# Kernel tuning notes

Hardware: AMD Instinct MI355X
Metric: run time of the kernel (lower is better)

## Reference

```python
import jax, jax.numpy as jnp
import numpy as np

N, E, D, H, C, ED, G = 50000, 1000000, 128, 8, 16, 16, 8
HC = H * C  # = output_dim = 128
EPS = 1e-5
NEG_SLOPE = 0.2


def setup_inputs() -> dict:
    key = jax.random.key(0)
    ks = jax.random.split(key, 12)
    s = 1.0 / np.sqrt(D)
    inp = {
        "x": jax.random.normal(ks[0], (N, D), jnp.float32),
        "edge_index": jax.random.randint(ks[1], (2, E), 0, N, jnp.int64),
        "edge_attr": jax.random.normal(ks[2], (E, ED), jnp.float32),
        "batch": jnp.sort(jax.random.randint(ks[3], (N,), 0, G, jnp.int64)),
        # GATv2Conv params
        "Wl": jax.random.normal(ks[4], (D, HC), jnp.float32) * s,
        "bl": jnp.zeros((HC,), jnp.float32),
        "Wr": jax.random.normal(ks[5], (D, HC), jnp.float32) * s,
        "br": jnp.zeros((HC,), jnp.float32),
        "We": jax.random.normal(ks[6], (ED, HC), jnp.float32) * (1.0 / np.sqrt(ED)),
        "att": jax.random.normal(ks[7], (H, C), jnp.float32) * (1.0 / np.sqrt(C)),
        "bias": jnp.zeros((HC,), jnp.float32),
        # GraphNorm params
        "gn_weight": jnp.ones((HC,), jnp.float32),
        "gn_bias": jnp.zeros((HC,), jnp.float32),
        "gn_mean_scale": jnp.ones((HC,), jnp.float32),
    }
    return inp


def reference(x, edge_index, edge_attr, batch, Wl, bl, Wr, br, We, att, bias,
              gn_weight, gn_bias, gn_mean_scale):
    src, dst = edge_index[0], edge_index[1]

    # --- add self-loops with edge_attr fill_value='mean' (PyG default) ---
    deg = jax.ops.segment_sum(jnp.ones((E,), jnp.float32), dst, num_segments=N)
    ea_mean = jax.ops.segment_sum(edge_attr, dst, num_segments=N) / jnp.maximum(deg, 1.0)[:, None]
    loop = jnp.arange(N, dtype=src.dtype)
    src2 = jnp.concatenate([src, loop])          # [E+N]
    dst2 = jnp.concatenate([dst, loop])          # [E+N]
    ea2 = jnp.concatenate([edge_attr, ea_mean])  # [E+N, ED]

    # --- GATv2 attention ---
    xl = (x @ Wl + bl).reshape(N, H, C)  # source transform
    xr = (x @ Wr + br).reshape(N, H, C)  # target transform
    ee = (ea2 @ We).reshape(-1, H, C)
    m = xl[src2] + xr[dst2] + ee                              # [E+N, H, C]
    e = jnp.einsum('ehc,hc->eh', jax.nn.leaky_relu(m, NEG_SLOPE), att)  # [E+N, H]

    # segment softmax over destination nodes (every node has a self-loop)
    emax = jax.ops.segment_max(e, dst2, num_segments=N)       # [N, H]
    ex = jnp.exp(e - emax[dst2])
    denom = jax.ops.segment_sum(ex, dst2, num_segments=N)     # [N, H]
    alpha = ex / denom[dst2]                                  # [E+N, H]

    agg = jax.ops.segment_sum(alpha[:, :, None] * xl[src2], dst2, num_segments=N)
    out = agg.reshape(N, HC) + bias

    # residual (res_connection is Identity since input_dim == output_dim)
    out = out + x

    # --- GraphNorm over batch segments ---
    cnt = jax.ops.segment_sum(jnp.ones((N,), jnp.float32), batch, num_segments=G)
    cnt = jnp.maximum(cnt, 1.0)[:, None]
    mean = jax.ops.segment_sum(out, batch, num_segments=G) / cnt   # [G, HC]
    sub = out - gn_mean_scale * mean[batch]
    var = jax.ops.segment_sum(sub * sub, batch, num_segments=G) / cnt
    out = gn_weight * sub / jnp.sqrt(var[batch] + EPS) + gn_bias

    # ELU activation (dropout is identity in eval)
    return jax.nn.elu(out)
```

## Files before the change

### kernel.cpp

```cpp
#include <hip/hip_runtime.h>

#define HC 128
#define HEADS 8
#define EDIM 16
#define NG 8
#define GEPS 1e-5f
#define LOG2E 1.44269504f

typedef float f32x2 __attribute__((ext_vector_type(2)));

__device__ __forceinline__ unsigned pack_bf16x2(float a, float b) {
  unsigned ua = __float_as_uint(a), ub = __float_as_uint(b);
  ua = (ua + 0x7fffu + ((ua >> 16) & 1u)) >> 16;
  ub = (ub + 0x7fffu + ((ub >> 16) & 1u)) >> 16;
  return ua | (ub << 16);
}
__device__ __forceinline__ f32x2 unpack_bf16x2(unsigned u) {
  return (f32x2){__uint_as_float(u << 16), __uint_as_float(u & 0xffff0000u)};
}

__device__ __forceinline__ float head8_sum(float p) {
  int t;
  t = __builtin_amdgcn_update_dpp(0, __float_as_int(p), 0x141, 0xF, 0xF, true);
  p += __int_as_float(t);
  t = __builtin_amdgcn_update_dpp(0, __float_as_int(p), 0x4E, 0xF, 0xF, true);
  p += __int_as_float(t);
  t = __builtin_amdgcn_update_dpp(0, __float_as_int(p), 0xB1, 0xF, 0xF, true);
  p += __int_as_float(t);
  return p;
}

__global__ void zero_k(float* __restrict__ p, size_t nwords) {
  size_t i = (size_t)blockIdx.x * 256 + threadIdx.x;
  if (i < nwords) p[i] = 0.f;
}

#define GEMM_ROWS 32
__global__ void __launch_bounds__(256) phase1(
    const float* __restrict__ x,
    const float* __restrict__ Wl, const float* __restrict__ bl,
    const float* __restrict__ Wr, const float* __restrict__ br,
    float* __restrict__ xr, unsigned* __restrict__ xlh,
    const int* __restrict__ ei, int* __restrict__ deg,
    const int* __restrict__ batch, int* __restrict__ genc,
    int nbG, int E, int N) {
  __shared__ float4 WL[32][32];
  __shared__ float4 WR[32][32];
  __shared__ float4 XS[GEMM_ROWS][8];
  int b = blockIdx.x;
  int t = threadIdx.x;
  if (b >= nbG) {
    int e = (b - nbG) * 256 + t;
    if (e >= E) return;
    atomicAdd(&deg[ei[E + e]], 1);
    if (e < N && (e == 0 || batch[e] != batch[e - 1])) {
      atomicMax(&genc[batch[e]], N - e);
    }
    return;
  }
  int cg = t & 31;
  int rt = t >> 5;
  int row0 = b * GEMM_ROWS;
  float4 bl4 = ((const float4*)bl)[cg];
  float4 br4 = ((const float4*)br)[cg];
  float4 accl[4], accr[4];
  #pragma unroll
  for (int r = 0; r < 4; ++r) { accl[r] = bl4; accr[r] = br4; }
  const float4* Wl4 = (const float4*)Wl;
  const float4* Wr4 = (const float4*)Wr;
  const float4* x4  = (const float4*)x;
  int srow = t >> 3, sk4 = t & 7;
  long sgrow = row0 + srow;
  for (int kc = 0; kc < 4; ++kc) {
    __syncthreads();
    #pragma unroll
    for (int i = 0; i < 4; ++i) {
      int idx = t + i * 256;
      int kr = idx >> 5, gg = idx & 31;
      WL[kr][gg] = Wl4[(kc * 32 + kr) * 32 + gg];
      WR[kr][gg] = Wr4[(kc * 32 + kr) * 32 + gg];
    }
    XS[srow][sk4] = (sgrow < N) ? x4[sgrow * 32 + kc * 8 + sk4]
                                : make_float4(0.f, 0.f, 0.f, 0.f);
    __syncthreads();
    #pragma unroll
    for (int k4 = 0; k4 < 8; ++k4) {
      float4 xv[4];
      #pragma unroll
      for (int r = 0; r < 4; ++r) xv[r] = XS[rt * 4 + r][k4];
      #pragma unroll
      for (int kk = 0; kk < 4; ++kk) {
        float4 wl = WL[k4 * 4 + kk][cg];
        float4 wr = WR[k4 * 4 + kk][cg];
        #pragma unroll
        for (int r = 0; r < 4; ++r) {
          float xs = (&xv[r].x)[kk];
          accl[r].x = fmaf(xs, wl.x, accl[r].x);
          accl[r].y = fmaf(xs, wl.y, accl[r].y);
          accl[r].z = fmaf(xs, wl.z, accl[r].z);
          accl[r].w = fmaf(xs, wl.w, accl[r].w);
          accr[r].x = fmaf(xs, wr.x, accr[r].x);
          accr[r].y = fmaf(xs, wr.y, accr[r].y);
          accr[r].z = fmaf(xs, wr.z, accr[r].z);
          accr[r].w = fmaf(xs, wr.w, accr[r].w);
        }
      }
    }
  }
  #pragma unroll
  for (int r = 0; r < 4; ++r) {
    long row = row0 + rt * 4 + r;
    if (row < N) {
      ((float4*)(xr + row * HC))[cg] = accr[r];
      uint2 h;
      h.x = pack_bf16x2(accl[r].x, accl[r].y);
      h.y = pack_bf16x2(accl[r].z, accl[r].w);
      ((uint2*)(xlh + row * (HC / 2)))[cg] = h;
    }
  }
}

__global__ void scan1(const int* __restrict__ deg, int* __restrict__ bsum, int N) {
  __shared__ int s[256];
  int t = threadIdx.x;
  int n = blockIdx.x * 256 + t;
  s[t] = (n < N) ? deg[n] : 0;
  __syncthreads();
  for (int off = 128; off > 0; off >>= 1) {
    if (t < off) s[t] += s[t + off];
    __syncthreads();
  }
  if (t == 0) bsum[blockIdx.x] = s[0];
}
__global__ void scan2(const int* __restrict__ bsum, int* __restrict__ bofs, int nb,
                      int* __restrict__ offsets, int N,
                      const int* __restrict__ genc, int* __restrict__ gstart) {
  __shared__ int s[256];
  int t = threadIdx.x;
  int v = (t < nb) ? bsum[t] : 0;
  s[t] = v;
  __syncthreads();
  for (int off = 1; off < 256; off <<= 1) {
    int add = (t >= off) ? s[t - off] : 0;
    __syncthreads();
    s[t] += add;
    __syncthreads();
  }
  if (t < nb) bofs[t] = s[t] - v;
  if (t == 255) offsets[N] = s[255];
  if (t == 0) {
    int nxt = N;
    gstart[NG] = N;
    for (int g = NG - 1; g >= 0; --g) {
      int st = N - genc[g];
      if (st > nxt) st = nxt;
      gstart[g] = st;
      nxt = st;
    }
  }
}
__global__ void scan3(const int* __restrict__ deg, const int* __restrict__ bofs,
                      int* __restrict__ offsets, int N) {
  __shared__ int s[256];
  int t = threadIdx.x;
  int n = blockIdx.x * 256 + t;
  int v = (n < N) ? deg[n] : 0;
  s[t] = v;
  __syncthreads();
  for (int off = 1; off < 256; off <<= 1) {
    int add = (t >= off) ? s[t - off] : 0;
    __syncthreads();
    s[t] += add;
    __syncthreads();
  }
  if (n < N) offsets[n] = bofs[blockIdx.x] + s[t] - v;
}

__global__ void fill_csr(const int* __restrict__ ei, int* __restrict__ deg,
                         const int* __restrict__ offsets, int2* __restrict__ csr2, int E) {
  int e = blockIdx.x * 256 + threadIdx.x;
  if (e >= E) return;
  int d = ei[E + e];
  int pos = atomicSub(&deg[d], 1) - 1;
  csr2[offsets[d] + pos] = make_int2(e, ei[e]);
}

__global__ void __launch_bounds__(64) fused_node(
    const int* __restrict__ offsets, const int2* __restrict__ csr2,
    const float* __restrict__ ea, const unsigned* __restrict__ xlh,
    const float* __restrict__ xr,
    const float* __restrict__ We, const float* __restrict__ att,
    const float* __restrict__ x, const float* __restrict__ bias,
    float* __restrict__ out, int N) {
  int l = threadIdx.x;
  long n = blockIdx.x;
  if (n >= N) return;
  int c0 = l * 2;
  f32x2 wx[8], wy[8];
  #pragma unroll
  for (int kp = 0; kp < 8; ++kp) {
    wx[kp] = (f32x2){We[(2 * kp) * HC + c0],     We[(2 * kp + 1) * HC + c0]};
    wy[kp] = (f32x2){We[(2 * kp) * HC + c0 + 1], We[(2 * kp + 1) * HC + c0 + 1]};
  }
  f32x2 av2 = {att[c0] * LOG2E, att[c0 + 1] * LOG2E};
  f32x2 av08 = 0.8f * av2, av02 = 0.2f * av2;
  f32x2 xl2 = unpack_bf16x2(xlh[n * (HC / 2) + l]);
  f32x2 xr2 = *(const f32x2*)(xr + n * HC + c0);
  f32x2 seedA = {xr2.x, 0.f};
  f32x2 seedB = {xr2.y, 0.f};
  int j0 = offsets[n], j1 = offsets[n + 1];

  float m = -INFINITY;
  float den = 0.f;
  f32x2 acc = {0.f, 0.f};
  f32x2 eesum = {0.f, 0.f};

  auto edge_update = [&](int e, f32x2 xls) {
    const float4* eap = (const float4*)(ea + (long)e * EDIM);
    float4 a0 = eap[0], a1 = eap[1], a2 = eap[2], a3 = eap[3];
    f32x2 dA = seedA, dB = seedB;
    f32x2 e01;
    e01 = (f32x2){a0.x, a0.y};
    dA = __builtin_elementwise_fma(e01, wx[0], dA);
    dB = __builtin_elementwise_fma(e01, wy[0], dB);
    e01 = (f32x2){a0.z, a0.w};
    dA = __builtin_elementwise_fma(e01, wx[1], dA);
    dB = __builtin_elementwise_fma(e01, wy[1], dB);
    e01 = (f32x2){a1.x, a1.y};
    dA = __builtin_elementwise_fma(e01, wx[2], dA);
    dB = __builtin_elementwise_fma(e01, wy[2], dB);
    e01 = (f32x2){a1.z, a1.w};
    dA = __builtin_elementwise_fma(e01, wx[3], dA);
    dB = __builtin_elementwise_fma(e01, wy[3], dB);
    e01 = (f32x2){a2.x, a2.y};
    dA = __builtin_elementwise_fma(e01, wx[4], dA);
    dB = __builtin_elementwise_fma(e01, wy[4], dB);
    e01 = (f32x2){a2.z, a2.w};
    dA = __builtin_elementwise_fma(e01, wx[5], dA);
    dB = __builtin_elementwise_fma(e01, wy[5], dB);
    e01 = (f32x2){a3.x, a3.y};
    dA = __builtin_elementwise_fma(e01, wx[6], dA);
    dB = __builtin_elementwise_fma(e01, wy[6], dB);
    e01 = (f32x2){a3.z, a3.w};
    dA = __builtin_elementwise_fma(e01, wx[7], dA);
    dB = __builtin_elementwise_fma(e01, wy[7], dB);
    f32x2 mm = {dA.x + dA.y, dB.x + dB.y};
    eesum += mm;
    mm += xls;
    f32x2 tt = __builtin_elementwise_fma(
        av08, __builtin_elementwise_max(mm, (f32x2)0.f), av02 * mm);
    float p = head8_sum(tt.x + tt.y);
    if (p > m + 11.5f) {
      float sc = exp2f(m - p);
      acc = acc * sc + xls;
      den = fmaf(den, sc, 1.f);
      m = p;
    } else {
      float w = exp2f(p - m);
      acc = __builtin_elementwise_fma((f32x2)w, xls, acc);
      den += w;
    }
  };

  auto gath = [&](int s) -> f32x2 {
    return unpack_bf16x2(xlh[(long)s * (HC / 2) + l]);
  };
  auto edge_single = [&](int jj) {
    int2 es = csr2[jj];
    int e = __builtin_amdgcn_readfirstlane(es.x);
    int s = __builtin_amdgcn_readfirstlane(es.y);
    edge_update(e, gath(s));
  };

  int j = j0;
  if ((j & 1) && j < j1) { edge_single(j); ++j; }
  for (; j + 1 < j1; j += 2) {
    int4 q = *(const int4*)(csr2 + j);
    int e0 = __builtin_amdgcn_readfirstlane(q.x);
    int s0 = __builtin_amdgcn_readfirstlane(q.y);
    int e1 = __builtin_amdgcn_readfirstlane(q.z);
    int s1 = __builtin_amdgcn_readfirstlane(q.w);
    f32x2 xls0 = gath(s0);
    f32x2 xls1 = gath(s1);
    edge_update(e0, xls0);
    edge_update(e1, xls1);
  }
  if (j < j1) edge_single(j);

  int dg = j1 - j0;
  f32x2 ee = (dg > 0) ? (eesum * (1.f / (float)dg) - xr2) : (f32x2)0.f;
  f32x2 mm = xl2 + xr2 + ee;
  f32x2 tt = __builtin_elementwise_fma(
      av08, __builtin_elementwise_max(mm, (f32x2)0.f), av02 * mm);
  float p = head8_sum(tt.x + tt.y);
  if (p > m) {
    float sc = exp2f(m - p);
    acc = acc * sc + xl2;
    den = fmaf(den, sc, 1.f);
  } else {
    float w = exp2f(p - m);
    acc = __builtin_elementwise_fma((f32x2)w, xl2, acc);
    den += w;
  }

  f32x2 b2 = *(const f32x2*)(bias + c0);
  f32x2 x2 = *(const f32x2*)(x + n * HC + c0);
  f32x2 o = acc * (1.f / den) + b2 + x2;
  *(f32x2*)(out + n * HC + c0) = o;
}

#define GN_SLICES 32
__global__ void __launch_bounds__(128) gn_stats(
    const float* __restrict__ out, const int* __restrict__ gstart,
    float* __restrict__ gsum, float* __restrict__ gsq) {
  int g = blockIdx.x >> 5;
  int slice = blockIdx.x & 31;
  int s0 = gstart[g], s1 = gstart[g + 1];
  int cnt = s1 - s0;
  if (cnt <= 0) return;
  int chunk = (cnt + GN_SLICES - 1) / GN_SLICES;
  int lo = s0 + slice * chunk;
  int hi = lo + chunk; if (hi > s1) hi = s1;
  if (lo >= hi) return;
  int ch = threadIdx.x;
  float sum = 0.f, sq = 0.f;
  for (int nrow = lo; nrow < hi; ++nrow) {
    float v = out[(long)nrow * HC + ch];
    sum += v; sq += v * v;
  }
  atomicAdd(&gsum[g * HC + ch], sum);
  atomicAdd(&gsq[g * HC + ch], sq);
}

__global__ void gn_apply(float* __restrict__ out, const int* __restrict__ batch,
                         const float* __restrict__ gsum, const float* __restrict__ gsq,
                         const int* __restrict__ gstart, const float* __restrict__ gms,
                         const float* __restrict__ gnw, const float* __restrict__ gnb, int N) {
  long i = (long)blockIdx.x * 256 + threadIdx.x;
  if (i >= (long)N * 32) return;
  int c4 = (int)(i & 31);
  long n = i >> 5;
  int g = batch[n];
  float cnt = (float)(gstart[g + 1] - gstart[g]);
  if (cnt < 1.f) cnt = 1.f;
  float ic = 1.f / cnt;
  float4 su = ((const float4*)gsum)[g * 32 + c4];
  float4 sq = ((const float4*)gsq)[g * 32 + c4];
  float4 ms4 = ((const float4*)gms)[c4];
  float4 v = ((const float4*)out)[i];
  float4 w  = ((const float4*)gnw)[c4];
  float4 b  = ((const float4*)gnb)[c4];
  float4 o;
  #pragma unroll
  for (int k = 0; k < 4; ++k) {
    float mean = (&su.x)[k] * ic;
    float c = (&ms4.x)[k] * mean;
    float var = (&sq.x)[k] * ic - 2.f * c * mean + c * c;
    float istd = rsqrtf(var + GEPS);
    float oo = fmaf((&w.x)[k] * ((&v.x)[k] - c), istd, (&b.x)[k]);
    (&o.x)[k] = oo > 0.f ? oo : expm1f(oo);
  }
  ((float4*)out)[i] = o;
}

extern "C" void kernel_launch(void* const* d_in, const int* in_sizes, int n_in,
                              void* d_out, int out_size, void* d_ws, size_t ws_size,
                              hipStream_t stream) {
  const float* x    = (const float*)d_in[0];
  const int*   ei   = (const int*)d_in[1];
  const float* ea   = (const float*)d_in[2];
  const int*   batch= (const int*)d_in[3];
  const float* Wl   = (const float*)d_in[4];
  const float* bl   = (const float*)d_in[5];
  const float* Wr   = (const float*)d_in[6];
  const float* br   = (const float*)d_in[7];
  const float* We   = (const float*)d_in[8];
  const float* att  = (const float*)d_in[9];
  const float* bias = (const float*)d_in[10];
  const float* gnw  = (const float*)d_in[11];
  const float* gnb  = (const float*)d_in[12];
  const float* gms  = (const float*)d_in[13];
  int N = in_sizes[0] / HC;
  int E = in_sizes[2] / EDIM;
  float* out = (float*)d_out;
  (void)n_in; (void)out_size; (void)ws_size;

  float* wsf = (float*)d_ws;
  size_t off = 0;
  auto alloc = [&](size_t words) -> float* {
    float* p = wsf + off;
    off += (words + 3) & ~(size_t)3;
    return p;
  };
  int*      deg     = (int*)alloc(N);
  float*    gsum    = alloc(NG * HC);
  float*    gsq     = alloc(NG * HC);
  int*      genc    = (int*)alloc(NG);
  size_t zero_words = off;
  int*      gstart  = (int*)alloc(NG + 1);
  int*      bsum    = (int*)alloc(256);
  int*      bofs    = (int*)alloc(256);
  int*      offsets = (int*)alloc((size_t)N + 1);
  float*    xr      = alloc((size_t)N * HC);
  unsigned* xlh     = (unsigned*)alloc((size_t)N * (HC / 2));
  int2*     csr2    = (int2*)alloc((size_t)E * 2 + 8);

  int nb = (N + 255) / 256;
  int nbG = (N + GEMM_ROWS - 1) / GEMM_ROWS;
  int nbC = (E + 255) / 256;

  zero_k<<<(unsigned)((zero_words + 255) / 256), 256, 0, stream>>>(wsf, zero_words);
  phase1<<<nbG + nbC, 256, 0, stream>>>(x, Wl, bl, Wr, br, xr, xlh,
                                        ei, deg, batch, genc, nbG, E, N);
  scan1<<<nb, 256, 0, stream>>>(deg, bsum, N);
  scan2<<<1, 256, 0, stream>>>(bsum, bofs, nb, offsets, N, genc, gstart);
  scan3<<<nb, 256, 0, stream>>>(deg, bofs, offsets, N);
  fill_csr<<<(E + 255) / 256, 256, 0, stream>>>(ei, deg, offsets, csr2, E);
  fused_node<<<N, 64, 0, stream>>>(offsets, csr2, ea, xlh, xr, We, att, x, bias, out, N);
  gn_stats<<<NG * GN_SLICES, 128, 0, stream>>>(out, gstart, gsum, gsq);
  {
    long tot = (long)N * 32;
    gn_apply<<<(unsigned)((tot + 255) / 256), 256, 0, stream>>>(out, batch, gsum, gsq, gstart, gms, gnw, gnb, N);
  }
}
```

Measured before the change: 328.7 us.

## Double GEMM rows per block and merge scan2/scan3 into one kernel

The projection GEMM tile grows from 32 to 64 rows per block, so each thread computes 8 rows and the shared weight tiles are reused across twice as many rows. Separately, the block-offset scan and the per-node offset scan are fused into one kernel where each block sums the preceding block totals itself, removing one launch. The cost is higher register pressure in phase1 and redundant prefix summation across blocks.

```diff
diff --git a/kernel.cpp b/kernel.cpp
--- a/kernel.cpp
+++ b/kernel.cpp
@@ -35,7 +35,7 @@
   if (i < nwords) p[i] = 0.f;
 }
 
-#define GEMM_ROWS 32
+#define GEMM_ROWS 64
 __global__ void __launch_bounds__(256) phase1(
     const float* __restrict__ x,
     const float* __restrict__ Wl, const float* __restrict__ bl,
@@ -63,14 +63,12 @@
   int row0 = b * GEMM_ROWS;
   float4 bl4 = ((const float4*)bl)[cg];
   float4 br4 = ((const float4*)br)[cg];
-  float4 accl[4], accr[4];
+  float4 accl[8], accr[8];
   #pragma unroll
-  for (int r = 0; r < 4; ++r) { accl[r] = bl4; accr[r] = br4; }
+  for (int r = 0; r < 8; ++r) { accl[r] = bl4; accr[r] = br4; }
   const float4* Wl4 = (const float4*)Wl;
   const float4* Wr4 = (const float4*)Wr;
   const float4* x4  = (const float4*)x;
-  int srow = t >> 3, sk4 = t & 7;
-  long sgrow = row0 + srow;
   for (int kc = 0; kc < 4; ++kc) {
     __syncthreads();
     #pragma unroll
@@ -80,20 +78,26 @@
       WL[kr][gg] = Wl4[(kc * 32 + kr) * 32 + gg];
       WR[kr][gg] = Wr4[(kc * 32 + kr) * 32 + gg];
     }
-    XS[srow][sk4] = (sgrow < N) ? x4[sgrow * 32 + kc * 8 + sk4]
-                                : make_float4(0.f, 0.f, 0.f, 0.f);
+    #pragma unroll
+    for (int i = 0; i < 2; ++i) {
+      int idx = t + i * 256;
+      int srow = idx >> 3, sk4 = idx & 7;
+      long sgrow = row0 + srow;
+      XS[srow][sk4] = (sgrow < N) ? x4[sgrow * 32 + kc * 8 + sk4]
+                                  : make_float4(0.f, 0.f, 0.f, 0.f);
+    }
     __syncthreads();
     #pragma unroll
     for (int k4 = 0; k4 < 8; ++k4) {
-      float4 xv[4];
+      float4 xv[8];
       #pragma unroll
-      for (int r = 0; r < 4; ++r) xv[r] = XS[rt * 4 + r][k4];
+      for (int r = 0; r < 8; ++r) xv[r] = XS[rt * 8 + r][k4];
       #pragma unroll
       for (int kk = 0; kk < 4; ++kk) {
         float4 wl = WL[k4 * 4 + kk][cg];
         float4 wr = WR[k4 * 4 + kk][cg];
         #pragma unroll
-        for (int r = 0; r < 4; ++r) {
+        for (int r = 0; r < 8; ++r) {
           float xs = (&xv[r].x)[kk];
           accl[r].x = fmaf(xs, wl.x, accl[r].x);
           accl[r].y = fmaf(xs, wl.y, accl[r].y);
@@ -108,8 +112,8 @@
     }
   }
   #pragma unroll
-  for (int r = 0; r < 4; ++r) {
-    long row = row0 + rt * 4 + r;
+  for (int r = 0; r < 8; ++r) {
+    long row = row0 + rt * 8 + r;
     if (row < N) {
       ((float4*)(xr + row * HC))[cg] = accr[r];
       uint2 h;
@@ -132,12 +136,28 @@
   }
   if (t == 0) bsum[blockIdx.x] = s[0];
 }
-__global__ void scan2(const int* __restrict__ bsum, int* __restrict__ bofs, int nb,
-                      int* __restrict__ offsets, int N,
-                      const int* __restrict__ genc, int* __restrict__ gstart) {
+
+__global__ void scan23(const int* __restrict__ deg, const int* __restrict__ bsum,
+                       int* __restrict__ offsets, int N, int nb,
+                       const int* __restrict__ genc, int* __restrict__ gstart) {
   __shared__ int s[256];
+  __shared__ int sprefix;
   int t = threadIdx.x;
-  int v = (t < nb) ? bsum[t] : 0;
+  int b = blockIdx.x;
+  int pre = 0;
+  for (int i = t; i < b; i += 256) pre += bsum[i];
+  s[t] = pre;
+  __syncthreads();
+  for (int off = 128; off > 0; off >>= 1) {
+    if (t < off) s[t] += s[t + off];
+    __syncthreads();
+  }
+  if (t == 0) sprefix = s[0];
+  __syncthreads();
+  int prefix = sprefix;
+  __syncthreads();
+  int n = b * 256 + t;
+  int v = (n < N) ? deg[n] : 0;
   s[t] = v;
   __syncthreads();
   for (int off = 1; off < 256; off <<= 1) {
@@ -146,9 +166,9 @@
     s[t] += add;
     __syncthreads();
   }
-  if (t < nb) bofs[t] = s[t] - v;
-  if (t == 255) offsets[N] = s[255];
-  if (t == 0) {
+  if (n < N) offsets[n] = prefix + s[t] - v;
+  if (b == nb - 1 && t == 255) offsets[N] = prefix + s[255];
+  if (b == 0 && t == 0) {
     int nxt = N;
     gstart[NG] = N;
     for (int g = NG - 1; g >= 0; --g) {
@@ -158,22 +178,6 @@
       nxt = st;
     }
   }
-}
-__global__ void scan3(const int* __restrict__ deg, const int* __restrict__ bofs,
-                      int* __restrict__ offsets, int N) {
-  __shared__ int s[256];
-  int t = threadIdx.x;
-  int n = blockIdx.x * 256 + t;
-  int v = (n < N) ? deg[n] : 0;
-  s[t] = v;
-  __syncthreads();
-  for (int off = 1; off < 256; off <<= 1) {
-    int add = (t >= off) ? s[t - off] : 0;
-    __syncthreads();
-    s[t] += add;
-    __syncthreads();
-  }
-  if (n < N) offsets[n] = bofs[blockIdx.x] + s[t] - v;
 }
 
 __global__ void fill_csr(const int* __restrict__ ei, int* __restrict__ deg,
@@ -399,7 +403,6 @@
   size_t zero_words = off;
   int*      gstart  = (int*)alloc(NG + 1);
   int*      bsum    = (int*)alloc(256);
-  int*      bofs    = (int*)alloc(256);
   int*      offsets = (int*)alloc((size_t)N + 1);
   float*    xr      = alloc((size_t)N * HC);
   unsigned* xlh     = (unsigned*)alloc((size_t)N * (HC / 2));
@@ -413,8 +416,7 @@
   phase1<<<nbG + nbC, 256, 0, stream>>>(x, Wl, bl, Wr, br, xr, xlh,
                                         ei, deg, batch, genc, nbG, E, N);
   scan1<<<nb, 256, 0, stream>>>(deg, bsum, N);
-  scan2<<<1, 256, 0, stream>>>(bsum, bofs, nb, offsets, N, genc, gstart);
-  scan3<<<nb, 256, 0, stream>>>(deg, bofs, offsets, N);
+  scan23<<<nb, 256, 0, stream>>>(deg, bsum, offsets, N, nb, genc, gstart);
   fill_csr<<<(E + 255) / 256, 256, 0, stream>>>(ei, deg, offsets, csr2, E);
   fused_node<<<N, 64, 0, stream>>>(offsets, csr2, ea, xlh, xr, We, att, x, bias, out, N);
   gn_stats<<<NG * GN_SLICES, 128, 0, stream>>>(out, gstart, gsum, gsq);
```

Result: faster. 320.0 us (-2.7%).
